# Optimization experiments

Hardware: AMD Instinct MI355X
Metric: run time of the kernel (lower is better)

Reference implementation:

```python
import jax, jax.numpy as jnp
import numpy as np

EPS = 1e-5

def mean_std_norm(x):
    # instance norm without affine: per-(B,C) mean/std over spatial dims
    mean = jnp.mean(x, axis=(2, 3), keepdims=True)
    var = jnp.var(x, axis=(2, 3), keepdims=True)
    return (x - mean) / jnp.sqrt(var + EPS)

def conv1x1(x, w, b):
    # x: [B,C,H,W], w: [O,C], b: [O]
    return jnp.einsum('oc,bchw->bohw', w, x) + b[None, :, None, None]

def setup_inputs() -> dict:
    key = jax.random.key(0)
    ks = jax.random.split(key, 9)
    C = 512
    s = 1.0 / np.sqrt(C)
    inp = {
        'content_feat': jax.random.normal(ks[0], (4, C, 64, 64), dtype=jnp.float32),
        'f_w': jax.random.normal(ks[1], (C, C), dtype=jnp.float32) * s,
        'f_b': jnp.zeros((C,), dtype=jnp.float32),
        'g_w': jax.random.normal(ks[2], (C, C), dtype=jnp.float32) * s,
        'g_b': jnp.zeros((C,), dtype=jnp.float32),
        'h_w': jax.random.normal(ks[3], (C, C), dtype=jnp.float32) * s,
        'h_b': jnp.zeros((C,), dtype=jnp.float32),
        'o_w': jax.random.normal(ks[4], (C, C), dtype=jnp.float32) * s,
        'o_b': jnp.zeros((C,), dtype=jnp.float32),
    }
    return inp

def reference(content_feat, f_w, f_b, g_w, g_b, h_w, h_b, o_w, o_b):
    B, C, H, W = content_feat.shape
    HW = H * W
    norm = mean_std_norm(content_feat)
    # f(norm) -> [B, HW, C]; g(norm) -> [B, C, HW]
    F_Fc = conv1x1(norm, f_w, f_b).reshape(B, C, HW).transpose(0, 2, 1)
    G_Fs = conv1x1(norm, g_w, g_b).reshape(B, C, HW)
    energy = jnp.einsum('bnc,bcm->bnm', F_Fc, G_Fs)  # [B, HW, HW]
    attention = jax.nn.softmax(energy, axis=-1)
    H_Fs = conv1x1(content_feat, h_w, h_b).reshape(B, C, HW)
    # out = H_Fs @ attention^T : out[b,c,m] = sum_n H_Fs[b,c,n] * att[b,m,n]
    out = jnp.einsum('bcn,bmn->bcm', H_Fs, attention).reshape(B, C, H, W)
    out = conv1x1(out, o_w, o_b)
    return out + content_feat
```

## Files before the change

### kernel.cpp

```cpp
#include <hip/hip_runtime.h>


typedef __bf16 bf16_t;
typedef __bf16 bf16x8 __attribute__((ext_vector_type(8)));
typedef _Float16 f16_t;
typedef _Float16 f16x8 __attribute__((ext_vector_type(8)));
typedef float f32x4 __attribute__((ext_vector_type(4)));

#define LOG2E 1.44269504088896340736f

__device__ __forceinline__ void gload16(const void* g, void* l) {
  __builtin_amdgcn_global_load_lds(
      (const __attribute__((address_space(1))) void*)g,
      (__attribute__((address_space(3))) void*)l, 16, 0, 0);
}

__global__ void __launch_bounds__(256) stats_k(const float* __restrict__ x,
                                               float* __restrict__ mu,
                                               float* __restrict__ rs) {
  const int bc = blockIdx.x;
  const float4* row = (const float4*)(x + (size_t)bc * 4096);
  float s = 0.f, ss = 0.f;
  for (int i = threadIdx.x; i < 1024; i += 256) {
    float4 v = row[i];
    s += v.x + v.y + v.z + v.w;
    ss += v.x * v.x + v.y * v.y + v.z * v.z + v.w * v.w;
  }
#pragma unroll
  for (int o = 32; o >= 1; o >>= 1) {
    s += __shfl_down(s, o);
    ss += __shfl_down(ss, o);
  }
  __shared__ float as_[4], ass_[4];
  const int w = threadIdx.x >> 6;
  if ((threadIdx.x & 63) == 0) { as_[w] = s; ass_[w] = ss; }
  __syncthreads();
  if (threadIdx.x == 0) {
    float st = as_[0] + as_[1] + as_[2] + as_[3];
    float sst = ass_[0] + ass_[1] + ass_[2] + ass_[3];
    float m = st * (1.f / 4096.f);
    float var = sst * (1.f / 4096.f) - m * m;
    mu[bc] = m;
    rs[bc] = rsqrtf(var + 1e-5f);
  }
}

__global__ void __launch_bounds__(256) wcast2_k(const float* __restrict__ a,
                                                const float* __restrict__ b,
                                                f16_t* __restrict__ dst) {
  const int i = blockIdx.x * 256 + threadIdx.x;
  const int which = i >> 16;
  const int off = i & 65535;
  const float* s = which ? b : a;
  const float4 v = ((const float4*)s)[off];
  alignas(8) f16_t r[4];
  r[0] = (f16_t)v.x; r[1] = (f16_t)v.y; r[2] = (f16_t)v.z; r[3] = (f16_t)v.w;
  *(uint2*)(dst + ((size_t)which << 18) + (size_t)off * 4) = *(const uint2*)r;
}

__global__ void __launch_bounds__(256) mt_k(const float* __restrict__ fw,
                                            const float* __restrict__ gw,
                                            bf16_t* __restrict__ Mth,
                                            bf16_t* __restrict__ Mtl) {
  __shared__ float Fs[32][64];
  __shared__ float Gs[32][64];
  const int t = threadIdx.x;
  const int it = blockIdx.x, jt = blockIdx.y;
  float acc[16];
#pragma unroll
  for (int i = 0; i < 16; ++i) acc[i] = 0.f;
  const int jl = t >> 2, ib = (t & 3) * 16;
  const int lr = t >> 4, lc4 = (t & 15) * 4;
  for (int cc = 0; cc < 16; ++cc) {
    __syncthreads();
#pragma unroll
    for (int rep = 0; rep < 2; ++rep) {
      const int r = lr + rep * 16;
      *(float4*)&Fs[r][lc4] = *(const float4*)(fw + (size_t)(cc * 32 + r) * 512 + it * 64 + lc4);
      *(float4*)&Gs[r][lc4] = *(const float4*)(gw + (size_t)(cc * 32 + r) * 512 + jt * 64 + lc4);
    }
    __syncthreads();
#pragma unroll
    for (int c = 0; c < 32; ++c) {
      const float gv = Gs[c][jl];
#pragma unroll
      for (int ii = 0; ii < 16; ++ii) acc[ii] += gv * Fs[c][ib + ii];
    }
  }
  alignas(16) bf16_t hi[16], lo[16];
#pragma unroll
  for (int ii = 0; ii < 16; ++ii) {
    hi[ii] = (bf16_t)acc[ii];
    lo[ii] = (bf16_t)(acc[ii] - (float)hi[ii]);
  }
  const size_t o = (size_t)(jt * 64 + jl) * 512 + it * 64 + ib;
  *(uint4*)(Mth + o) = *(const uint4*)hi;
  *(uint4*)(Mth + o + 8) = *(const uint4*)(hi + 8);
  *(uint4*)(Mtl + o) = *(const uint4*)lo;
  *(uint4*)(Mtl + o + 8) = *(const uint4*)(lo + 8);
}

__global__ void __launch_bounds__(256) v_k(const float* __restrict__ gw,
                                           const float* __restrict__ fb,
                                           float* __restrict__ v) {
  const int j = blockIdx.x * 256 + threadIdx.x;
  float s = 0.f;
  for (int c = 0; c < 512; ++c) s += gw[(size_t)c * 512 + j] * fb[c];
  v[j] = s;
}

__global__ void __launch_bounds__(256) u_k(const float* __restrict__ v,
                                           const bf16_t* __restrict__ xnh,
                                           const bf16_t* __restrict__ xnl,
                                           float* __restrict__ u) {
  const int w = threadIdx.x >> 6, lane = threadIdx.x & 63;
  const int m = blockIdx.x * 4 + w;
  const int b = blockIdx.y;
  const size_t o = ((size_t)b * 4096 + m) * 512 + lane * 8;
  const bf16x8 vh = *(const bf16x8*)(xnh + o);
  const bf16x8 vl = *(const bf16x8*)(xnl + o);
  const float4 v0 = *(const float4*)(v + lane * 8);
  const float4 v1 = *(const float4*)(v + lane * 8 + 4);
  float s = 0.f;
  const float* vp = &v0.x;
#pragma unroll
  for (int e = 0; e < 4; ++e) s += ((float)vh[e] + (float)vl[e]) * vp[e];
  const float* vq = &v1.x;
#pragma unroll
  for (int e = 0; e < 4; ++e) s += ((float)vh[4 + e] + (float)vl[4 + e]) * vq[e];
#pragma unroll
  for (int o2 = 32; o2 >= 1; o2 >>= 1) s += __shfl_down(s, o2);
  if (lane == 0) u[(size_t)b * 4096 + m] = s;
}

__global__ void __launch_bounds__(256) normt_k(const float* __restrict__ x,
                                               const float* __restrict__ mu,
                                               const float* __restrict__ rs,
                                               bf16_t* __restrict__ xnh,
                                               bf16_t* __restrict__ xnl,
                                               f16_t* __restrict__ xf,
                                               f16_t* __restrict__ xc) {
  __shared__ float tile[64][65];
  const int t = threadIdx.x;
  const int nt = blockIdx.x, ct = blockIdx.y, b = blockIdx.z;
  const float* src = x + ((size_t)b * 512 + ct * 64) * 4096 + nt * 64;
  {
    const int r = t >> 4, cq = (t & 15) * 4;
#pragma unroll
    for (int it = 0; it < 4; ++it) {
      const int rr = r + it * 16;
      const float4 v = *(const float4*)(src + (size_t)rr * 4096 + cq);
      tile[rr][cq] = v.x; tile[rr][cq + 1] = v.y;
      tile[rr][cq + 2] = v.z; tile[rr][cq + 3] = v.w;
    }
  }
  __syncthreads();
  const int n = t & 63, ch = t >> 6;
  alignas(16) bf16_t vh[16], vl[16];
  alignas(16) f16_t vf[16], vc[16];
#pragma unroll
  for (int i = 0; i < 16; ++i) {
    const int c = ch * 16 + i;
    const float v = tile[c][n];
    const int gc = b * 512 + ct * 64 + c;
    vc[i] = (f16_t)v;
    const float vn = (v - mu[gc]) * rs[gc];
    const bf16_t h = (bf16_t)vn;
    vh[i] = h;
    vl[i] = (bf16_t)(vn - (float)h);
    vf[i] = (f16_t)vn;
  }
  const size_t o = ((size_t)b * 4096 + nt * 64 + n) * 512 + ct * 64 + ch * 16;
  *(uint4*)(xnh + o) = *(const uint4*)vh;
  *(uint4*)(xnh + o + 8) = *(const uint4*)(vh + 8);
  *(uint4*)(xnl + o) = *(const uint4*)vl;
  *(uint4*)(xnl + o + 8) = *(const uint4*)(vl + 8);
  *(uint4*)(xf + o) = *(const uint4*)vf;
  *(uint4*)(xf + o + 8) = *(const uint4*)(vf + 8);
  *(uint4*)(xc + o) = *(const uint4*)vc;
  *(uint4*)(xc + o + 8) = *(const uint4*)(vc + 8);
}

template <typename OT, int BIAS, bool RESID>
__global__ void __launch_bounds__(256) gemm_k(const f16_t* __restrict__ A,
                                              const f16_t* __restrict__ Bt,
                                              OT* __restrict__ C,
                                              const float* __restrict__ biasM,
                                              const float* __restrict__ biasN,
                                              const float* __restrict__ resid,
                                              long sAb, long sBb, long sCb, int ldC) {
  __shared__ alignas(16) f16_t As[2][128 * 64];
  __shared__ alignas(16) f16_t Bs[2][128 * 64];
  const int t = threadIdx.x;
  const int lane = t & 63;
  const int w = t >> 6;
  const int wr = w >> 1, wc = w & 1;
  const int l15 = lane & 15, lg = lane >> 4;
  const int b = blockIdx.z;
  const int m0 = blockIdx.y * 128, n0 = blockIdx.x * 128;
  const f16_t* Ab = A + (size_t)sAb * b + (size_t)m0 * 512;
  const f16_t* Bb = Bt + (size_t)sBb * b + (size_t)n0 * 512;
  const int srow = t >> 3;
  const int slot = t & 7;

  auto gstage = [&](int pb_, int ks_) {
#pragma unroll
    for (int r_ = 0; r_ < 4; ++r_) {
      const int rr_ = r_ * 32 + srow;
      const size_t go_ = (size_t)rr_ * 512 + ks_ * 64 + ((slot ^ (rr_ & 7)) * 8);
      gload16(Ab + go_, (char*)As[pb_] + r_ * 4096 + w * 1024);
      gload16(Bb + go_, (char*)Bs[pb_] + r_ * 4096 + w * 1024);
    }
  };

  const f32x4 z4 = {0.f, 0.f, 0.f, 0.f};
  f32x4 acc[4][4];
#pragma unroll
  for (int i = 0; i < 4; ++i)
#pragma unroll
    for (int j = 0; j < 4; ++j) acc[i][j] = z4;

  gstage(0, 0);
  __syncthreads();
  for (int ks = 0; ks < 8; ++ks) {
    const int pb = ks & 1;
    if (ks < 7) gstage(pb ^ 1, ks + 1);
#pragma unroll
    for (int kk = 0; kk < 2; ++kk) {
      f16x8 af[4], bfr[4];
#pragma unroll
      for (int i = 0; i < 4; ++i) {
        const int ra = wr * 64 + i * 16 + l15;
        af[i] = *(const f16x8*)((const char*)As[pb] + ra * 128 + (((kk * 4 + lg) ^ (ra & 7)) * 16));
        const int rb = wc * 64 + i * 16 + l15;
        bfr[i] = *(const f16x8*)((const char*)Bs[pb] + rb * 128 + (((kk * 4 + lg) ^ (rb & 7)) * 16));
      }
#pragma unroll
      for (int i = 0; i < 4; ++i)
#pragma unroll
        for (int j = 0; j < 4; ++j)
          acc[i][j] = __builtin_amdgcn_mfma_f32_16x16x32_f16(af[i], bfr[j], acc[i][j], 0, 0, 0);
    }
    __syncthreads();
  }
  OT* Cb = C + (size_t)sCb * b;
#pragma unroll
  for (int i = 0; i < 4; ++i) {
#pragma unroll
    for (int j = 0; j < 4; ++j) {
      const int n = n0 + wc * 64 + j * 16 + l15;
      float bn = 0.f;
      if (BIAS == 2) bn = biasN[n];
#pragma unroll
      for (int r = 0; r < 4; ++r) {
        const int m = m0 + wr * 64 + i * 16 + lg * 4 + r;
        float v = acc[i][j][r] + bn;
        if (BIAS == 1) v += biasM[m];
        if (RESID) v += resid[(size_t)sCb * b + (size_t)m * ldC + n];
        Cb[(size_t)m * ldC + n] = (OT)v;
      }
    }
  }
}

__global__ void __launch_bounds__(256) gemm3_k(const bf16_t* __restrict__ Ah,
                                               const bf16_t* __restrict__ Al,
                                               const bf16_t* __restrict__ Bh,
                                               const bf16_t* __restrict__ Bl,
                                               f16_t* __restrict__ Cf,
                                               long sAb, long sCb) {
  __shared__ alignas(16) bf16_t Ash[2][128 * 64];
  __shared__ alignas(16) bf16_t Asl[2][128 * 64];
  __shared__ alignas(16) bf16_t Bsh[2][128 * 64];
  __shared__ alignas(16) bf16_t Bsl[2][128 * 64];
  const int t = threadIdx.x;
  const int lane = t & 63;
  const int w = t >> 6;
  const int wr = w >> 1, wc = w & 1;
  const int l15 = lane & 15, lg = lane >> 4;
  const int b = blockIdx.z;
  const int m0 = blockIdx.y * 128, n0 = blockIdx.x * 128;
  const bf16_t* Ahb = Ah + (size_t)sAb * b + (size_t)m0 * 512;
  const bf16_t* Alb = Al + (size_t)sAb * b + (size_t)m0 * 512;
  const bf16_t* Bhb = Bh + (size_t)n0 * 512;
  const bf16_t* Blb = Bl + (size_t)n0 * 512;
  const int srow = t >> 3;
  const int slot = t & 7;

  auto gstage = [&](int pb_, int ks_) {
#pragma unroll
    for (int r_ = 0; r_ < 4; ++r_) {
      const int rr_ = r_ * 32 + srow;
      const size_t go_ = (size_t)rr_ * 512 + ks_ * 64 + ((slot ^ (rr_ & 7)) * 8);
      gload16(Ahb + go_, (char*)Ash[pb_] + r_ * 4096 + w * 1024);
      gload16(Alb + go_, (char*)Asl[pb_] + r_ * 4096 + w * 1024);
      gload16(Bhb + go_, (char*)Bsh[pb_] + r_ * 4096 + w * 1024);
      gload16(Blb + go_, (char*)Bsl[pb_] + r_ * 4096 + w * 1024);
    }
  };

  const f32x4 z4 = {0.f, 0.f, 0.f, 0.f};
  f32x4 acc[4][4];
#pragma unroll
  for (int i = 0; i < 4; ++i)
#pragma unroll
    for (int j = 0; j < 4; ++j) acc[i][j] = z4;

  gstage(0, 0);
  __syncthreads();
  for (int ks = 0; ks < 8; ++ks) {
    const int pb = ks & 1;
    if (ks < 7) gstage(pb ^ 1, ks + 1);
#pragma unroll
    for (int kk = 0; kk < 2; ++kk) {
      bf16x8 ah[4], al[4], bh[4], bl[4];
#pragma unroll
      for (int i = 0; i < 4; ++i) {
        const int ra = wr * 64 + i * 16 + l15;
        const int sa = (((kk * 4 + lg) ^ (ra & 7)) * 16);
        ah[i] = *(const bf16x8*)((const char*)Ash[pb] + ra * 128 + sa);
        al[i] = *(const bf16x8*)((const char*)Asl[pb] + ra * 128 + sa);
        const int rb = wc * 64 + i * 16 + l15;
        const int sb = (((kk * 4 + lg) ^ (rb & 7)) * 16);
        bh[i] = *(const bf16x8*)((const char*)Bsh[pb] + rb * 128 + sb);
        bl[i] = *(const bf16x8*)((const char*)Bsl[pb] + rb * 128 + sb);
      }
#pragma unroll
      for (int i = 0; i < 4; ++i)
#pragma unroll
        for (int j = 0; j < 4; ++j) {
          acc[i][j] = __builtin_amdgcn_mfma_f32_16x16x32_bf16(ah[i], bh[j], acc[i][j], 0, 0, 0);
          acc[i][j] = __builtin_amdgcn_mfma_f32_16x16x32_bf16(ah[i], bl[j], acc[i][j], 0, 0, 0);
          acc[i][j] = __builtin_amdgcn_mfma_f32_16x16x32_bf16(al[i], bh[j], acc[i][j], 0, 0, 0);
        }
    }
    __syncthreads();
  }
  f16_t* Cfb = Cf + (size_t)sCb * b;
#pragma unroll
  for (int i = 0; i < 4; ++i) {
#pragma unroll
    for (int j = 0; j < 4; ++j) {
      const int n = n0 + wc * 64 + j * 16 + l15;
#pragma unroll
      for (int r = 0; r < 4; ++r) {
        const int m = m0 + wr * 64 + i * 16 + lg * 4 + r;
        Cfb[(size_t)m * 512 + n] = (f16_t)acc[i][j][r];
      }
    }
  }
}

__global__ void __launch_bounds__(512, 2) flash_k(const f16_t* __restrict__ Z,
                                                  const f16_t* __restrict__ X,
                                                  const float* __restrict__ u,
                                                  const f16_t* __restrict__ Hv,
                                                  f16_t* __restrict__ Oat_t) {
  __shared__ alignas(16) f16_t K[2][64 * 256];
  __shared__ alignas(16) f16_t P[64 * 64];
  __shared__ float ulds[4096];
  __shared__ float redm[4][2][16];
  __shared__ float reds[4][2][16];
  __shared__ float alds[64];
  __shared__ float llds[64];

  const int t = threadIdx.x;
  const int lane = t & 63;
  const int w = t >> 6;
  const int wq = w & 3, wk = w >> 2;
  const int l15 = lane & 15, lg = lane >> 4;
  const int bid = blockIdx.x;
  const int xcd = bid & 7;
  const int b = xcd >> 1;
  const int q0 = ((xcd & 1) * 32 + (bid >> 3)) * 64;

  const f16_t* Kb = X + (size_t)b * 4096 * 512;
  const f16_t* Vb = Hv + (size_t)b * 512 * 4096;
  const float* ub = u + (size_t)b * 4096;

  const int srow = w * 2 + (lane >> 5);
  const int slot32 = lane & 31;

  auto stagek = [&](int pb_, int kt_, int hf_) {
    const int k0_ = kt_ * 64;
#pragma unroll
    for (int r_ = 0; r_ < 4; ++r_) {
      const int row_ = r_ * 16 + srow;
      const size_t go_ = (size_t)(k0_ + row_) * 512 + hf_ * 256 + ((slot32 ^ (row_ & 7)) * 8);
      gload16(Kb + go_, (char*)K[pb_] + r_ * 8192 + w * 1024);
    }
  };

#define QKHALF(PB, HF)                                                                        \
  do {                                                                                        \
    _Pragma("unroll") for (int cwl_ = 0; cwl_ < 8; ++cwl_) {                                  \
      const f16x8 qf_ = qf[(HF) * 8 + cwl_];                                                  \
      _Pragma("unroll") for (int mf_ = 0; mf_ < 2; ++mf_) {                                   \
        const int key_ = 32 * wk + 16 * mf_ + l15;                                            \
        const int so_ = ((cwl_ * 4 + lg) ^ (key_ & 7)) * 16;                                  \
        const f16x8 kf_ = *(const f16x8*)((const char*)K[PB] + key_ * 512 + so_);             \
        sacc[mf_] = __builtin_amdgcn_mfma_f32_16x16x32_f16(kf_, qf_, sacc[mf_], 0, 0, 0);     \
      }                                                                                       \
    }                                                                                         \
  } while (0)

  f16x8 qf[16];
  {
    const size_t qo = ((size_t)b * 4096 + q0 + 16 * wq + l15) * 512 + lg * 8;
#pragma unroll
    for (int cw = 0; cw < 16; ++cw) qf[cw] = *(const f16x8*)(Z + qo + cw * 32);
  }
#pragma unroll
  for (int r = 0; r < 2; ++r)
    gload16(ub + r * 2048 + t * 4, (char*)ulds + r * 8192 + w * 1024);
  stagek(0, 0, 0);

  const f32x4 z4 = {0.f, 0.f, 0.f, 0.f};
  f32x4 oacc[4][4];
#pragma unroll
  for (int i = 0; i < 4; ++i)
#pragma unroll
    for (int j = 0; j < 4; ++j) oacc[i][j] = z4;
  float m_run = -3.0e38f, l_run = 0.f;

  __syncthreads();

  for (int kt = 0; kt < 64; ++kt) {
    const int k0 = kt * 64;
    f32x4 sacc[2] = {z4, z4};
    stagek(1, kt, 1);
    QKHALF(0, 0);
    __syncthreads();
    if (kt < 63) stagek(0, kt + 1, 0);
    f16x8 vpre[4][2];
#pragma unroll
    for (int ct = 0; ct < 4; ++ct) {
      const int c = 64 * w + 16 * ct + l15;
#pragma unroll
      for (int kk = 0; kk < 2; ++kk)
        vpre[ct][kk] = *(const f16x8*)(Vb + (size_t)c * 4096 + k0 + kk * 32 + lg * 8);
    }
    QKHALF(1, 1);
    float pm = -3.0e38f;
#pragma unroll
    for (int mf = 0; mf < 2; ++mf)
#pragma unroll
      for (int j = 0; j < 4; ++j) {
        sacc[mf][j] += ulds[k0 + 32 * wk + 16 * mf + 4 * lg + j];
        pm = fmaxf(pm, sacc[mf][j]);
      }
    pm = fmaxf(pm, __shfl_xor(pm, 16));
    pm = fmaxf(pm, __shfl_xor(pm, 32));
    if (lane < 16) redm[wq][wk][lane] = pm;
    __syncthreads();
    const float m_tile = fmaxf(pm, redm[wq][wk ^ 1][l15]);
    const float m_new = fmaxf(m_run, m_tile);
    const float alpha = exp2f((m_run - m_new) * LOG2E);
    m_run = m_new;
    float ps = 0.f;
    const int qrow = 16 * wq + l15;
    {
      alignas(8) f16_t pk[4];
#pragma unroll
      for (int mf = 0; mf < 2; ++mf) {
#pragma unroll
        for (int j = 0; j < 4; ++j) {
          const float p = exp2f((sacc[mf][j] - m_new) * LOG2E);
          ps += p;
          pk[j] = (f16_t)p;
        }
        const int byo = qrow * 128 + ((64 * wk + 32 * mf + 8 * lg) ^ ((qrow & 7) << 4));
        *(uint2*)((char*)P + byo) = *(const uint2*)pk;
      }
    }
    ps += __shfl_xor(ps, 16);
    ps += __shfl_xor(ps, 32);
    if (lane < 16) {
      reds[wq][wk][lane] = ps;
      if (wk == 0) alds[16 * wq + lane] = alpha;
    }
    __syncthreads();
    const float s_tile = reds[wq][0][l15] + reds[wq][1][l15];
    l_run = l_run * alpha + s_tile;
    float aq[4];
#pragma unroll
    for (int qt = 0; qt < 4; ++qt) aq[qt] = alds[16 * qt + l15];
#pragma unroll
    for (int ct = 0; ct < 4; ++ct)
#pragma unroll
      for (int qt = 0; qt < 4; ++qt) oacc[ct][qt] *= aq[qt];
#pragma unroll
    for (int kk = 0; kk < 2; ++kk) {
      f16x8 bp[4];
#pragma unroll
      for (int qt = 0; qt < 4; ++qt) {
        const int q = 16 * qt + l15;
        bp[qt] = *(const f16x8*)((const char*)P + q * 128 +
                                 ((kk * 64 + lg * 16) ^ ((q & 7) << 4)));
      }
#pragma unroll
      for (int ct = 0; ct < 4; ++ct)
#pragma unroll
        for (int qt = 0; qt < 4; ++qt)
          oacc[ct][qt] =
              __builtin_amdgcn_mfma_f32_16x16x32_f16(vpre[ct][kk], bp[qt], oacc[ct][qt], 0, 0, 0);
    }
  }
#undef QKHALF
  if (wk == 0 && lane < 16) llds[16 * wq + lane] = l_run;
  __syncthreads();
  float inv[4];
#pragma unroll
  for (int qt = 0; qt < 4; ++qt) inv[qt] = 1.f / llds[16 * qt + l15];
#pragma unroll
  for (int ct = 0; ct < 4; ++ct)
#pragma unroll
    for (int qt = 0; qt < 4; ++qt) {
      alignas(8) f16_t o4[4];
#pragma unroll
      for (int j = 0; j < 4; ++j) o4[j] = (f16_t)(oacc[ct][qt][j] * inv[qt]);
      *(uint2*)(Oat_t + ((size_t)b * 4096 + q0 + 16 * qt + l15) * 512 + 64 * w + 16 * ct + 4 * lg) =
          *(const uint2*)o4;
    }
}

extern "C" void kernel_launch(void* const* d_in, const int* in_sizes, int n_in,
                              void* d_out, int out_size, void* d_ws, size_t ws_size,
                              hipStream_t stream) {
  const float* x = (const float*)d_in[0];
  const float* fw = (const float*)d_in[1];
  const float* fb = (const float*)d_in[2];
  const float* gw = (const float*)d_in[3];
  const float* gb = (const float*)d_in[4];
  const float* hw = (const float*)d_in[5];
  const float* hb = (const float*)d_in[6];
  const float* ow = (const float*)d_in[7];
  const float* ob = (const float*)d_in[8];
  float* out = (float*)d_out;
  (void)gb;

  const size_t BIG = (size_t)4 * 4096 * 512 * sizeof(bf16_t);
  char* p = (char*)d_ws;
  float* mu = (float*)p; p += 2048 * sizeof(float);
  float* rs = (float*)p; p += 2048 * sizeof(float);
  float* vv = (float*)p; p += 512 * sizeof(float);
  float* uu = (float*)p; p += (size_t)4 * 4096 * sizeof(float);
  f16_t* w2 = (f16_t*)p; p += (size_t)2 * 512 * 512 * sizeof(f16_t);
  bf16_t* Mth = (bf16_t*)p; p += (size_t)512 * 512 * sizeof(bf16_t);
  bf16_t* Mtl = (bf16_t*)p; p += (size_t)512 * 512 * sizeof(bf16_t);
  bf16_t* xnh = (bf16_t*)p; p += BIG;
  bf16_t* xnl = (bf16_t*)p; p += BIG;
  f16_t* xf = (f16_t*)p; p += BIG;
  f16_t* xc = (f16_t*)p; p += BIG;
  f16_t* Zf = (f16_t*)p; p += BIG;
  f16_t* Hv = (f16_t*)p; p += BIG;
  f16_t* Oat_t = xc;

  f16_t* whb = w2;
  f16_t* wob = w2 + 262144;

  const long sD = (long)4096 * 512;

  stats_k<<<2048, 256, 0, stream>>>(x, mu, rs);
  wcast2_k<<<512, 256, 0, stream>>>(hw, ow, w2);
  mt_k<<<dim3(8, 8), 256, 0, stream>>>(fw, gw, Mth, Mtl);
  v_k<<<2, 256, 0, stream>>>(gw, fb, vv);
  normt_k<<<dim3(64, 8, 4), 256, 0, stream>>>(x, mu, rs, xnh, xnl, xf, xc);
  u_k<<<dim3(1024, 4), 256, 0, stream>>>(vv, xnh, xnl, uu);
  gemm3_k<<<dim3(4, 32, 4), 256, 0, stream>>>(xnh, xnl, Mth, Mtl, Zf, sD, sD);
  gemm_k<f16_t, 1, false><<<dim3(32, 4, 4), 256, 0, stream>>>(
      whb, xc, Hv, hb, nullptr, nullptr, 0, sD, sD, 4096);
  flash_k<<<256, 512, 0, stream>>>(Zf, xf, uu, Hv, Oat_t);
  gemm_k<float, 1, true><<<dim3(32, 4, 4), 256, 0, stream>>>(
      wob, Oat_t, out, ob, nullptr, x, 0, sD, sD, 4096);

  (void)in_sizes; (void)n_in; (void)out_size; (void)ws_size;
}
```

Baseline: 425.4 us.

## Drop bf16 split-precision Z GEMM for fp16 and re-pipeline flash attention loop

Replaces the three-pass bf16 hi/lo split GEMM for Z = Xn·M with a single fp16 GEMM through the generic gemm_k, and removes the xnh/xnl buffers and their writes. The flash kernel loads u directly from global instead of staging it in LDS, and double-buffers K staging with explicit waitcnt, barriers and setprio. It also pads P rows instead of XOR-swizzling them. Output rescaling is skipped unless the running max grows by more than 8, which lowers exp and multiply work but risks fp16 overflow and lost accuracy in the energy values.

```diff
diff --git a/kernel.cpp b/kernel.cpp
--- a/kernel.cpp
+++ b/kernel.cpp
@@ -2,7 +2,6 @@
 
 
 typedef __bf16 bf16_t;
-typedef __bf16 bf16x8 __attribute__((ext_vector_type(8)));
 typedef _Float16 f16_t;
 typedef _Float16 f16x8 __attribute__((ext_vector_type(8)));
 typedef float f32x4 __attribute__((ext_vector_type(4)));
@@ -14,6 +13,12 @@
       (const __attribute__((address_space(1))) void*)g,
       (__attribute__((address_space(3))) void*)l, 16, 0, 0);
 }
+
+#define WAITV14() asm volatile("s_waitcnt vmcnt(14)" ::: "memory")
+#define WAITV10() asm volatile("s_waitcnt vmcnt(10)" ::: "memory")
+#define WAITL() asm volatile("s_waitcnt lgkmcnt(0)" ::: "memory")
+#define SB() __builtin_amdgcn_s_barrier()
+#define SCHED0() __builtin_amdgcn_sched_barrier(0)
 
 __global__ void __launch_bounds__(256) stats_k(const float* __restrict__ x,
                                                float* __restrict__ mu,
@@ -60,8 +65,7 @@
 
 __global__ void __launch_bounds__(256) mt_k(const float* __restrict__ fw,
                                             const float* __restrict__ gw,
-                                            bf16_t* __restrict__ Mth,
-                                            bf16_t* __restrict__ Mtl) {
+                                            f16_t* __restrict__ Mh) {
   __shared__ float Fs[32][64];
   __shared__ float Gs[32][64];
   const int t = threadIdx.x;
@@ -87,17 +91,12 @@
       for (int ii = 0; ii < 16; ++ii) acc[ii] += gv * Fs[c][ib + ii];
     }
   }
-  alignas(16) bf16_t hi[16], lo[16];
-#pragma unroll
-  for (int ii = 0; ii < 16; ++ii) {
-    hi[ii] = (bf16_t)acc[ii];
-    lo[ii] = (bf16_t)(acc[ii] - (float)hi[ii]);
-  }
+  alignas(16) f16_t hi[16];
+#pragma unroll
+  for (int ii = 0; ii < 16; ++ii) hi[ii] = (f16_t)acc[ii];
   const size_t o = (size_t)(jt * 64 + jl) * 512 + it * 64 + ib;
-  *(uint4*)(Mth + o) = *(const uint4*)hi;
-  *(uint4*)(Mth + o + 8) = *(const uint4*)(hi + 8);
-  *(uint4*)(Mtl + o) = *(const uint4*)lo;
-  *(uint4*)(Mtl + o + 8) = *(const uint4*)(lo + 8);
+  *(uint4*)(Mh + o) = *(const uint4*)hi;
+  *(uint4*)(Mh + o + 8) = *(const uint4*)(hi + 8);
 }
 
 __global__ void __launch_bounds__(256) v_k(const float* __restrict__ gw,
@@ -110,24 +109,22 @@
 }
 
 __global__ void __launch_bounds__(256) u_k(const float* __restrict__ v,
-                                           const bf16_t* __restrict__ xnh,
-                                           const bf16_t* __restrict__ xnl,
+                                           const f16_t* __restrict__ xf,
                                            float* __restrict__ u) {
   const int w = threadIdx.x >> 6, lane = threadIdx.x & 63;
   const int m = blockIdx.x * 4 + w;
   const int b = blockIdx.y;
   const size_t o = ((size_t)b * 4096 + m) * 512 + lane * 8;
-  const bf16x8 vh = *(const bf16x8*)(xnh + o);
-  const bf16x8 vl = *(const bf16x8*)(xnl + o);
+  const f16x8 vh = *(const f16x8*)(xf + o);
   const float4 v0 = *(const float4*)(v + lane * 8);
   const float4 v1 = *(const float4*)(v + lane * 8 + 4);
   float s = 0.f;
   const float* vp = &v0.x;
 #pragma unroll
-  for (int e = 0; e < 4; ++e) s += ((float)vh[e] + (float)vl[e]) * vp[e];
+  for (int e = 0; e < 4; ++e) s += (float)vh[e] * vp[e];
   const float* vq = &v1.x;
 #pragma unroll
-  for (int e = 0; e < 4; ++e) s += ((float)vh[4 + e] + (float)vl[4 + e]) * vq[e];
+  for (int e = 0; e < 4; ++e) s += (float)vh[4 + e] * vq[e];
 #pragma unroll
   for (int o2 = 32; o2 >= 1; o2 >>= 1) s += __shfl_down(s, o2);
   if (lane == 0) u[(size_t)b * 4096 + m] = s;
@@ -136,8 +133,6 @@
 __global__ void __launch_bounds__(256) normt_k(const float* __restrict__ x,
                                                const float* __restrict__ mu,
                                                const float* __restrict__ rs,
-                                               bf16_t* __restrict__ xnh,
-                                               bf16_t* __restrict__ xnl,
                                                f16_t* __restrict__ xf,
                                                f16_t* __restrict__ xc) {
   __shared__ float tile[64][65];
@@ -156,7 +151,6 @@
   }
   __syncthreads();
   const int n = t & 63, ch = t >> 6;
-  alignas(16) bf16_t vh[16], vl[16];
   alignas(16) f16_t vf[16], vc[16];
 #pragma unroll
   for (int i = 0; i < 16; ++i) {
@@ -164,17 +158,9 @@
     const float v = tile[c][n];
     const int gc = b * 512 + ct * 64 + c;
     vc[i] = (f16_t)v;
-    const float vn = (v - mu[gc]) * rs[gc];
-    const bf16_t h = (bf16_t)vn;
-    vh[i] = h;
-    vl[i] = (bf16_t)(vn - (float)h);
-    vf[i] = (f16_t)vn;
+    vf[i] = (f16_t)((v - mu[gc]) * rs[gc]);
   }
   const size_t o = ((size_t)b * 4096 + nt * 64 + n) * 512 + ct * 64 + ch * 16;
-  *(uint4*)(xnh + o) = *(const uint4*)vh;
-  *(uint4*)(xnh + o + 8) = *(const uint4*)(vh + 8);
-  *(uint4*)(xnl + o) = *(const uint4*)vl;
-  *(uint4*)(xnl + o + 8) = *(const uint4*)(vl + 8);
   *(uint4*)(xf + o) = *(const uint4*)vf;
   *(uint4*)(xf + o + 8) = *(const uint4*)(vf + 8);
   *(uint4*)(xc + o) = *(const uint4*)vc;
@@ -263,102 +249,13 @@
   }
 }
 
-__global__ void __launch_bounds__(256) gemm3_k(const bf16_t* __restrict__ Ah,
-                                               const bf16_t* __restrict__ Al,
-                                               const bf16_t* __restrict__ Bh,
-                                               const bf16_t* __restrict__ Bl,
-                                               f16_t* __restrict__ Cf,
-                                               long sAb, long sCb) {
-  __shared__ alignas(16) bf16_t Ash[2][128 * 64];
-  __shared__ alignas(16) bf16_t Asl[2][128 * 64];
-  __shared__ alignas(16) bf16_t Bsh[2][128 * 64];
-  __shared__ alignas(16) bf16_t Bsl[2][128 * 64];
-  const int t = threadIdx.x;
-  const int lane = t & 63;
-  const int w = t >> 6;
-  const int wr = w >> 1, wc = w & 1;
-  const int l15 = lane & 15, lg = lane >> 4;
-  const int b = blockIdx.z;
-  const int m0 = blockIdx.y * 128, n0 = blockIdx.x * 128;
-  const bf16_t* Ahb = Ah + (size_t)sAb * b + (size_t)m0 * 512;
-  const bf16_t* Alb = Al + (size_t)sAb * b + (size_t)m0 * 512;
-  const bf16_t* Bhb = Bh + (size_t)n0 * 512;
-  const bf16_t* Blb = Bl + (size_t)n0 * 512;
-  const int srow = t >> 3;
-  const int slot = t & 7;
-
-  auto gstage = [&](int pb_, int ks_) {
-#pragma unroll
-    for (int r_ = 0; r_ < 4; ++r_) {
-      const int rr_ = r_ * 32 + srow;
-      const size_t go_ = (size_t)rr_ * 512 + ks_ * 64 + ((slot ^ (rr_ & 7)) * 8);
-      gload16(Ahb + go_, (char*)Ash[pb_] + r_ * 4096 + w * 1024);
-      gload16(Alb + go_, (char*)Asl[pb_] + r_ * 4096 + w * 1024);
-      gload16(Bhb + go_, (char*)Bsh[pb_] + r_ * 4096 + w * 1024);
-      gload16(Blb + go_, (char*)Bsl[pb_] + r_ * 4096 + w * 1024);
-    }
-  };
-
-  const f32x4 z4 = {0.f, 0.f, 0.f, 0.f};
-  f32x4 acc[4][4];
-#pragma unroll
-  for (int i = 0; i < 4; ++i)
-#pragma unroll
-    for (int j = 0; j < 4; ++j) acc[i][j] = z4;
-
-  gstage(0, 0);
-  __syncthreads();
-  for (int ks = 0; ks < 8; ++ks) {
-    const int pb = ks & 1;
-    if (ks < 7) gstage(pb ^ 1, ks + 1);
-#pragma unroll
-    for (int kk = 0; kk < 2; ++kk) {
-      bf16x8 ah[4], al[4], bh[4], bl[4];
-#pragma unroll
-      for (int i = 0; i < 4; ++i) {
-        const int ra = wr * 64 + i * 16 + l15;
-        const int sa = (((kk * 4 + lg) ^ (ra & 7)) * 16);
-        ah[i] = *(const bf16x8*)((const char*)Ash[pb] + ra * 128 + sa);
-        al[i] = *(const bf16x8*)((const char*)Asl[pb] + ra * 128 + sa);
-        const int rb = wc * 64 + i * 16 + l15;
-        const int sb = (((kk * 4 + lg) ^ (rb & 7)) * 16);
-        bh[i] = *(const bf16x8*)((const char*)Bsh[pb] + rb * 128 + sb);
-        bl[i] = *(const bf16x8*)((const char*)Bsl[pb] + rb * 128 + sb);
-      }
-#pragma unroll
-      for (int i = 0; i < 4; ++i)
-#pragma unroll
-        for (int j = 0; j < 4; ++j) {
-          acc[i][j] = __builtin_amdgcn_mfma_f32_16x16x32_bf16(ah[i], bh[j], acc[i][j], 0, 0, 0);
-          acc[i][j] = __builtin_amdgcn_mfma_f32_16x16x32_bf16(ah[i], bl[j], acc[i][j], 0, 0, 0);
-          acc[i][j] = __builtin_amdgcn_mfma_f32_16x16x32_bf16(al[i], bh[j], acc[i][j], 0, 0, 0);
-        }
-    }
-    __syncthreads();
-  }
-  f16_t* Cfb = Cf + (size_t)sCb * b;
-#pragma unroll
-  for (int i = 0; i < 4; ++i) {
-#pragma unroll
-    for (int j = 0; j < 4; ++j) {
-      const int n = n0 + wc * 64 + j * 16 + l15;
-#pragma unroll
-      for (int r = 0; r < 4; ++r) {
-        const int m = m0 + wr * 64 + i * 16 + lg * 4 + r;
-        Cfb[(size_t)m * 512 + n] = (f16_t)acc[i][j][r];
-      }
-    }
-  }
-}
-
 __global__ void __launch_bounds__(512, 2) flash_k(const f16_t* __restrict__ Z,
                                                   const f16_t* __restrict__ X,
                                                   const float* __restrict__ u,
                                                   const f16_t* __restrict__ Hv,
                                                   f16_t* __restrict__ Oat_t) {
   __shared__ alignas(16) f16_t K[2][64 * 256];
-  __shared__ alignas(16) f16_t P[64 * 64];
-  __shared__ float ulds[4096];
+  __shared__ alignas(16) f16_t P[64 * 72];
   __shared__ float redm[4][2][16];
   __shared__ float reds[4][2][16];
   __shared__ float alds[64];
@@ -410,10 +307,8 @@
 #pragma unroll
     for (int cw = 0; cw < 16; ++cw) qf[cw] = *(const f16x8*)(Z + qo + cw * 32);
   }
-#pragma unroll
-  for (int r = 0; r < 2; ++r)
-    gload16(ub + r * 2048 + t * 4, (char*)ulds + r * 8192 + w * 1024);
   stagek(0, 0, 0);
+  stagek(1, 0, 1);
 
   const f32x4 z4 = {0.f, 0.f, 0.f, 0.f};
   f32x4 oacc[4][4];
@@ -423,15 +318,12 @@
     for (int j = 0; j < 4; ++j) oacc[i][j] = z4;
   float m_run = -3.0e38f, l_run = 0.f;
 
-  __syncthreads();
-
   for (int kt = 0; kt < 64; ++kt) {
     const int k0 = kt * 64;
+    const int ktn = (kt + 1) & 63;
     f32x4 sacc[2] = {z4, z4};
-    stagek(1, kt, 1);
-    QKHALF(0, 0);
-    __syncthreads();
-    if (kt < 63) stagek(0, kt + 1, 0);
+    const float4 u0 = *(const float4*)(ub + k0 + 32 * wk + 4 * lg);
+    const float4 u1 = *(const float4*)(ub + k0 + 32 * wk + 16 + 4 * lg);
     f16x8 vpre[4][2];
 #pragma unroll
     for (int ct = 0; ct < 4; ++ct) {
@@ -440,23 +332,39 @@
       for (int kk = 0; kk < 2; ++kk)
         vpre[ct][kk] = *(const f16x8*)(Vb + (size_t)c * 4096 + k0 + kk * 32 + lg * 8);
     }
+    WAITV14(); WAITL(); SB(); SCHED0();
+    __builtin_amdgcn_s_setprio(1);
+    QKHALF(0, 0);
+    __builtin_amdgcn_s_setprio(0);
+    WAITL(); WAITV10(); SB(); SCHED0();
+    stagek(0, ktn, 0);
+    __builtin_amdgcn_s_setprio(1);
     QKHALF(1, 1);
+    __builtin_amdgcn_s_setprio(0);
     float pm = -3.0e38f;
-#pragma unroll
-    for (int mf = 0; mf < 2; ++mf)
+    {
+      const float* up0 = &u0.x;
+      const float* up1 = &u1.x;
 #pragma unroll
       for (int j = 0; j < 4; ++j) {
-        sacc[mf][j] += ulds[k0 + 32 * wk + 16 * mf + 4 * lg + j];
-        pm = fmaxf(pm, sacc[mf][j]);
+        sacc[0][j] += up0[j];
+        sacc[1][j] += up1[j];
+        pm = fmaxf(pm, fmaxf(sacc[0][j], sacc[1][j]));
       }
+    }
     pm = fmaxf(pm, __shfl_xor(pm, 16));
     pm = fmaxf(pm, __shfl_xor(pm, 32));
     if (lane < 16) redm[wq][wk][lane] = pm;
-    __syncthreads();
+    WAITL(); SB(); SCHED0();
+    stagek(1, ktn, 1);
     const float m_tile = fmaxf(pm, redm[wq][wk ^ 1][l15]);
-    const float m_new = fmaxf(m_run, m_tile);
-    const float alpha = exp2f((m_run - m_new) * LOG2E);
-    m_run = m_new;
+    float alpha;
+    if (m_tile > m_run + 8.f) {
+      alpha = exp2f((m_run - m_tile) * LOG2E);
+      m_run = m_tile;
+    } else {
+      alpha = 1.f;
+    }
     float ps = 0.f;
     const int qrow = 16 * wq + l15;
     {
@@ -465,12 +373,11 @@
       for (int mf = 0; mf < 2; ++mf) {
 #pragma unroll
         for (int j = 0; j < 4; ++j) {
-          const float p = exp2f((sacc[mf][j] - m_new) * LOG2E);
+          const float p = exp2f((sacc[mf][j] - m_run) * LOG2E);
           ps += p;
           pk[j] = (f16_t)p;
         }
-        const int byo = qrow * 128 + ((64 * wk + 32 * mf + 8 * lg) ^ ((qrow & 7) << 4));
-        *(uint2*)((char*)P + byo) = *(const uint2*)pk;
+        *(uint2*)((char*)P + qrow * 144 + 64 * wk + 32 * mf + 8 * lg) = *(const uint2*)pk;
       }
     }
     ps += __shfl_xor(ps, 16);
@@ -479,24 +386,27 @@
       reds[wq][wk][lane] = ps;
       if (wk == 0) alds[16 * wq + lane] = alpha;
     }
-    __syncthreads();
+    WAITL(); SB(); SCHED0();
     const float s_tile = reds[wq][0][l15] + reds[wq][1][l15];
     l_run = l_run * alpha + s_tile;
     float aq[4];
 #pragma unroll
     for (int qt = 0; qt < 4; ++qt) aq[qt] = alds[16 * qt + l15];
-#pragma unroll
-    for (int ct = 0; ct < 4; ++ct)
-#pragma unroll
-      for (int qt = 0; qt < 4; ++qt) oacc[ct][qt] *= aq[qt];
+    const bool need = (aq[0] != 1.f) || (aq[1] != 1.f) || (aq[2] != 1.f) || (aq[3] != 1.f);
+    if (__any(need)) {
+#pragma unroll
+      for (int ct = 0; ct < 4; ++ct)
+#pragma unroll
+        for (int qt = 0; qt < 4; ++qt) oacc[ct][qt] *= aq[qt];
+    }
+    __builtin_amdgcn_s_setprio(1);
 #pragma unroll
     for (int kk = 0; kk < 2; ++kk) {
       f16x8 bp[4];
 #pragma unroll
       for (int qt = 0; qt < 4; ++qt) {
         const int q = 16 * qt + l15;
-        bp[qt] = *(const f16x8*)((const char*)P + q * 128 +
-                                 ((kk * 64 + lg * 16) ^ ((q & 7) << 4)));
+        bp[qt] = *(const f16x8*)((const char*)P + q * 144 + kk * 64 + lg * 16);
       }
 #pragma unroll
       for (int ct = 0; ct < 4; ++ct)
@@ -505,6 +415,7 @@
           oacc[ct][qt] =
               __builtin_amdgcn_mfma_f32_16x16x32_f16(vpre[ct][kk], bp[qt], oacc[ct][qt], 0, 0, 0);
     }
+    __builtin_amdgcn_s_setprio(0);
   }
 #undef QKHALF
   if (wk == 0 && lane < 16) llds[16 * wq + lane] = l_run;
@@ -539,17 +450,14 @@
   float* out = (float*)d_out;
   (void)gb;
 
-  const size_t BIG = (size_t)4 * 4096 * 512 * sizeof(bf16_t);
+  const size_t BIG = (size_t)4 * 4096 * 512 * sizeof(f16_t);
   char* p = (char*)d_ws;
   float* mu = (float*)p; p += 2048 * sizeof(float);
   float* rs = (float*)p; p += 2048 * sizeof(float);
   float* vv = (float*)p; p += 512 * sizeof(float);
   float* uu = (float*)p; p += (size_t)4 * 4096 * sizeof(float);
   f16_t* w2 = (f16_t*)p; p += (size_t)2 * 512 * 512 * sizeof(f16_t);
-  bf16_t* Mth = (bf16_t*)p; p += (size_t)512 * 512 * sizeof(bf16_t);
-  bf16_t* Mtl = (bf16_t*)p; p += (size_t)512 * 512 * sizeof(bf16_t);
-  bf16_t* xnh = (bf16_t*)p; p += BIG;
-  bf16_t* xnl = (bf16_t*)p; p += BIG;
+  f16_t* Mh = (f16_t*)p; p += (size_t)512 * 512 * sizeof(f16_t);
   f16_t* xf = (f16_t*)p; p += BIG;
   f16_t* xc = (f16_t*)p; p += BIG;
   f16_t* Zf = (f16_t*)p; p += BIG;
@@ -563,11 +471,12 @@
 
   stats_k<<<2048, 256, 0, stream>>>(x, mu, rs);
   wcast2_k<<<512, 256, 0, stream>>>(hw, ow, w2);
-  mt_k<<<dim3(8, 8), 256, 0, stream>>>(fw, gw, Mth, Mtl);
+  mt_k<<<dim3(8, 8), 256, 0, stream>>>(fw, gw, Mh);
   v_k<<<2, 256, 0, stream>>>(gw, fb, vv);
-  normt_k<<<dim3(64, 8, 4), 256, 0, stream>>>(x, mu, rs, xnh, xnl, xf, xc);
-  u_k<<<dim3(1024, 4), 256, 0, stream>>>(vv, xnh, xnl, uu);
-  gemm3_k<<<dim3(4, 32, 4), 256, 0, stream>>>(xnh, xnl, Mth, Mtl, Zf, sD, sD);
+  normt_k<<<dim3(64, 8, 4), 256, 0, stream>>>(x, mu, rs, xf, xc);
+  u_k<<<dim3(1024, 4), 256, 0, stream>>>(vv, xf, uu);
+  gemm_k<f16_t, 0, false><<<dim3(4, 32, 4), 256, 0, stream>>>(
+      xf, Mh, Zf, nullptr, nullptr, nullptr, sD, 0, sD, 512);
   gemm_k<f16_t, 1, false><<<dim3(32, 4, 4), 256, 0, stream>>>(
       whb, xc, Hv, hb, nullptr, nullptr, 0, sD, sD, 4096);
   flash_k<<<256, 512, 0, stream>>>(Zf, xf, uu, Hv, Oat_t);
```

After: 404.1 us. 5.0% less time.
